# Kernel optimization log

Measured on AMD Instinct MI355X. Metric: run time of the kernel, lower is better.

Reference implementation:

```python
import jax, jax.numpy as jnp
import numpy as np
import math

D_MODEL = 1024
D_STATE = 16
D_CONV = 4
EXPAND = 2
D_INNER = EXPAND * D_MODEL
DT_RANK = math.ceil(D_MODEL / 16)
EPS = 1e-5


def setup_inputs() -> dict:
    key = jax.random.key(0)
    ks = jax.random.split(key, 8)
    B, L = 2, 1024
    s = 0.02
    return {
        "hidden_states": jax.random.normal(ks[0], (B, L, D_MODEL), jnp.float32),
        "norm_weight": jnp.ones((D_MODEL,), jnp.float32),
        "in_proj_w": (jax.random.normal(ks[1], (2 * D_INNER, D_MODEL), jnp.float32) * s),
        "conv_w": (jax.random.normal(ks[2], (D_INNER, D_CONV), jnp.float32) * s),
        "conv_b": jnp.zeros((D_INNER,), jnp.float32),
        "x_proj_w": (jax.random.normal(ks[3], (DT_RANK + 2 * D_STATE, D_INNER), jnp.float32) * s),
        "dt_proj_w": (jax.random.normal(ks[4], (D_INNER, DT_RANK), jnp.float32) * s),
        "dt_proj_b": jax.random.uniform(ks[5], (D_INNER,), jnp.float32, -4.0, -2.0),
        "A_log": jnp.log(jnp.broadcast_to(jnp.arange(1, D_STATE + 1, dtype=jnp.float32), (D_INNER, D_STATE))),
        "D": jnp.ones((D_INNER,), jnp.float32),
        "out_proj_w": (jax.random.normal(ks[6], (D_MODEL, D_INNER), jnp.float32) * s),
    }


def _rmsnorm(x, w):
    # Faithful to source: rms = ||x||_2 / sqrt(d); x / (rms + eps) * w
    norm = jnp.linalg.norm(x, axis=-1, keepdims=True)
    rms = norm * (1.0 / math.sqrt(x.shape[-1]))
    return w * (x / (rms + EPS))


def _mamba(h, in_proj_w, conv_w, conv_b, x_proj_w, dt_proj_w, dt_proj_b, A_log, D, out_proj_w):
    B, L, _ = h.shape
    xz = h @ in_proj_w.T                      # (B,L,2*D_INNER)
    x, z = jnp.split(xz, 2, axis=-1)          # each (B,L,D_INNER)

    # causal depthwise conv1d along L, kernel D_CONV
    xpad = jnp.pad(x, ((0, 0), (D_CONV - 1, 0), (0, 0)))
    xc = conv_b
    for k in range(D_CONV):                   # tiny fixed loop over kernel taps
        xc = xc + xpad[:, k:k + L, :] * conv_w[:, k]
    xc = jax.nn.silu(xc)                      # (B,L,D_INNER)

    x_dbl = xc @ x_proj_w.T                   # (B,L,DT_RANK+2N)
    dt, Bm, Cm = jnp.split(x_dbl, [DT_RANK, DT_RANK + D_STATE], axis=-1)
    dt = jax.nn.softplus(dt @ dt_proj_w.T + dt_proj_b)   # (B,L,D_INNER)

    A = -jnp.exp(A_log)                       # (D_INNER,N)
    deltaA = jnp.exp(dt[..., None] * A)                      # (B,L,D_INNER,N)
    deltaBu = (dt * xc)[..., None] * Bm[:, :, None, :]        # (B,L,D_INNER,N)

    def step(hst, inp):
        dA, dBu, Ct = inp
        hst = dA * hst + dBu                  # (B,D_INNER,N)
        y = jnp.einsum('bdn,bn->bd', hst, Ct)
        return hst, y

    h0 = jnp.zeros((B, D_INNER, D_STATE), xc.dtype)
    _, ys = jax.lax.scan(step, h0, (deltaA.swapaxes(0, 1), deltaBu.swapaxes(0, 1), Cm.swapaxes(0, 1)))
    y = ys.swapaxes(0, 1)                     # (B,L,D_INNER)
    y = y + D * xc
    y = y * jax.nn.silu(z)
    return y @ out_proj_w.T                   # (B,L,D_MODEL)


def reference(hidden_states, norm_weight, in_proj_w, conv_w, conv_b, x_proj_w,
              dt_proj_w, dt_proj_b, A_log, D, out_proj_w):
    residual = hidden_states
    h = _rmsnorm(residual, norm_weight)
    out = _mamba(h, in_proj_w, conv_w, conv_b, x_proj_w, dt_proj_w, dt_proj_b,
                 A_log, D, out_proj_w)
    return out, residual
```

## Files before the change

kernel.cpp:

```cpp
#include <hip/hip_runtime.h>

typedef __bf16 bf16x8 __attribute__((ext_vector_type(8)));
typedef float f32x4 __attribute__((ext_vector_type(4)));

__device__ __forceinline__ float b2f(ushort u) {
    union { unsigned int i; float f; } v;
    v.i = ((unsigned int)u) << 16;
    return v.f;
}
__device__ __forceinline__ ushort f2b(float f) {
    union { float f; unsigned int i; } v;
    v.f = f;
    unsigned int x = v.i;
    unsigned int r = (x + 0x7fffu + ((x >> 16) & 1u)) >> 16;
    return (ushort)r;
}
__device__ __forceinline__ float fexp2(float x) {
#if __has_builtin(__builtin_amdgcn_exp2f)
    return __builtin_amdgcn_exp2f(x);
#else
    return exp2f(x);
#endif
}
__device__ __forceinline__ void gload16(const ushort* g, ushort* l) {
    __builtin_amdgcn_global_load_lds(
        (const __attribute__((address_space(1))) unsigned int*)g,
        (__attribute__((address_space(3))) unsigned int*)l, 16, 0, 0);
}
__device__ __forceinline__ bf16x8 ldsfrag(const ushort* s, int row, int cq) {
    int p = cq ^ (row & 7);
    return *(const bf16x8*)(s + row * 64 + p * 8);
}

#define D_MODEL 1024
#define D_INNER 2048
#define D_STATE 16
#define DT_RANK 64
#define NTOK    2048
#define LSEQ    1024
#define NCH     64
#define LC      16
#define KSL     16
#define LOG2E   1.44269504088896f

__global__ __launch_bounds__(256) void prep_kernel(
    const float* __restrict__ hs, const float* __restrict__ w,
    ushort* __restrict__ hout, float* __restrict__ resid,
    const float* __restrict__ inproj, const float* __restrict__ outproj,
    const float* __restrict__ xprojw, const float* __restrict__ dtw,
    ushort* __restrict__ wIn, ushort* __restrict__ wOut,
    ushort* __restrict__ xpw, ushort* __restrict__ dtwb,
    float* __restrict__ xdbl)
{
    int blk = blockIdx.x;
    int tid = threadIdx.x;
    if (blk < NTOK) {
        int t = blk;
        float4 r4 = *(const float4*)(hs + (size_t)t * D_MODEL + tid * 4);
        float s = r4.x * r4.x + r4.y * r4.y + r4.z * r4.z + r4.w * r4.w;
        #pragma unroll
        for (int off = 32; off >= 1; off >>= 1) s += __shfl_xor(s, off);
        __shared__ float red[4];
        int lane = tid & 63, wid = tid >> 6;
        if (lane == 0) red[wid] = s;
        __syncthreads();
        float tot = red[0] + red[1] + red[2] + red[3];
        float inv = 1.0f / (sqrtf(tot) * (1.0f / 32.0f) + 1e-5f);
        float4 w4 = *(const float4*)(w + tid * 4);
        ushort4 o;
        o.x = f2b(w4.x * r4.x * inv);
        o.y = f2b(w4.y * r4.y * inv);
        o.z = f2b(w4.z * r4.z * inv);
        o.w = f2b(w4.w * r4.w * inv);
        *(ushort4*)(hout + (size_t)t * D_MODEL + tid * 4) = o;
        *(float4*)(resid + (size_t)t * D_MODEL + tid * 4) = r4;
    } else if (blk < NTOK + 6464) {
        int i = (blk - NTOK) * 256 + tid;
        const float* src; ushort* dst; int off;
        if (i < 1048576)      { src = inproj;  dst = wIn;  off = i; }
        else if (i < 1572864) { src = outproj; dst = wOut; off = i - 1048576; }
        else if (i < 1622016) { src = xprojw;  dst = xpw;  off = i - 1572864; }
        else if (i < 1654784) { src = dtw;     dst = dtwb; off = i - 1622016; }
        else return;
        float4 v = *(const float4*)(src + (size_t)off * 4);
        ushort4 o;
        o.x = f2b(v.x); o.y = f2b(v.y); o.z = f2b(v.z); o.w = f2b(v.w);
        *(ushort4*)(dst + (size_t)off * 4) = o;
    } else {
        int i = (blk - NTOK - 6464) * 256 + tid;
        if (i < 49152)
            *(float4*)(xdbl + (size_t)i * 4) = (float4){0.f, 0.f, 0.f, 0.f};
    }
}

__global__ __launch_bounds__(256) void gemm_xz_kernel(
    const ushort* __restrict__ Ag, const ushort* __restrict__ Wg,
    ushort* __restrict__ xq, ushort* __restrict__ zq, int K)
{
    __shared__ __align__(16) ushort smem[128 * 128];
    ushort* sA = smem;
    ushort* sB = smem + 128 * 64;
    int tid = threadIdx.x;
    int bm = blockIdx.x, bn = blockIdx.y;
    int wid = tid >> 6, lane = tid & 63;
    int wm = (wid >> 1) * 64, wn = (wid & 1) * 64;
    int l16 = lane & 15, q = lane >> 4;

    f32x4 acc[4][4];
    #pragma unroll
    for (int i = 0; i < 4; i++)
        #pragma unroll
        for (int j = 0; j < 4; j++)
            acc[i][j] = (f32x4){0.f, 0.f, 0.f, 0.f};

    const ushort* Abase = Ag + (size_t)bm * 128 * K;
    const ushort* Wbase = Wg + (size_t)bn * 128 * K;

    int segr = lane >> 3, segc = lane & 7;
    size_t goff[4]; int sseg[4];
    #pragma unroll
    for (int t = 0; t < 4; t++) {
        int s = wid * 4 + t;
        int r = s * 8 + segr;
        int gc = segc ^ (r & 7);
        sseg[t] = s * 512;
        goff[t] = (size_t)r * K + gc * 8;
    }

    for (int k0 = 0; k0 < K; k0 += 64) {
        __syncthreads();
        #pragma unroll
        for (int t = 0; t < 4; t++) {
            gload16(Abase + goff[t] + k0, sA + sseg[t]);
            gload16(Wbase + goff[t] + k0, sB + sseg[t]);
        }
        __syncthreads();
        #pragma unroll
        for (int ks = 0; ks < 2; ks++) {
            int cq = ks * 4 + q;
            bf16x8 af[4], bfr[4];
            #pragma unroll
            for (int i = 0; i < 4; i++)
                af[i] = ldsfrag(sA, wm + i * 16 + l16, cq);
            #pragma unroll
            for (int j = 0; j < 4; j++)
                bfr[j] = ldsfrag(sB, wn + j * 16 + l16, cq);
            #pragma unroll
            for (int i = 0; i < 4; i++)
                #pragma unroll
                for (int j = 0; j < 4; j++)
                    acc[i][j] = __builtin_amdgcn_mfma_f32_16x16x32_bf16(af[i], bfr[j], acc[i][j], 0, 0, 0);
        }
    }

    __syncthreads();
    #pragma unroll
    for (int i = 0; i < 4; i++)
        #pragma unroll
        for (int j = 0; j < 4; j++) {
            int col = wn + j * 16 + l16;
            int cchunk = col >> 3, cin = col & 7;
            #pragma unroll
            for (int r = 0; r < 4; r++) {
                int row = wm + i * 16 + q * 4 + r;
                smem[row * 128 + ((cchunk ^ (row & 7)) << 3) + cin] =
                    f2b(acc[i][j][r]);
            }
        }
    __syncthreads();
    ushort* dst = (bn < 16) ? xq : zq;
    int colbase = (bn & 15) * 128;
    size_t rowbase = (size_t)bm * 128;
    #pragma unroll
    for (int it = 0; it < 8; it++) {
        int flat = it * 2048 + tid * 8;
        int row = flat >> 7, cchunk = (flat & 127) >> 3;
        *(uint4*)(dst + (rowbase + row) * D_INNER + colbase + (cchunk << 3)) =
            *(const uint4*)(smem + row * 128 + ((cchunk ^ (row & 7)) << 3));
    }
}

__global__ __launch_bounds__(256) void gemm64_kernel(
    const ushort* __restrict__ Ag, const ushort* __restrict__ Wg,
    float* __restrict__ Cf, int M, int N, int K)
{
    __shared__ __align__(16) ushort smem[64 * 128];
    ushort* sA = smem;
    ushort* sB = smem + 64 * 64;
    float* fs = (float*)smem;
    int tid = threadIdx.x;
    int bm = blockIdx.x, bn = blockIdx.y;
    int wid = tid >> 6, lane = tid & 63;
    int wm = wid * 16;
    int l16 = lane & 15, q = lane >> 4;

    f32x4 acc[4];
    #pragma unroll
    for (int j = 0; j < 4; j++) acc[j] = (f32x4){0.f, 0.f, 0.f, 0.f};

    const ushort* Abase = Ag + (size_t)bm * 64 * K;
    const ushort* Wbase = Wg + (size_t)bn * 64 * K;

    int segr = lane >> 3, segc = lane & 7;
    size_t goff[2]; int sseg[2];
    #pragma unroll
    for (int t = 0; t < 2; t++) {
        int s = wid * 2 + t;
        int r = s * 8 + segr;
        int gc = segc ^ (r & 7);
        sseg[t] = s * 512;
        goff[t] = (size_t)r * K + gc * 8;
    }

    for (int k0 = 0; k0 < K; k0 += 64) {
        __syncthreads();
        #pragma unroll
        for (int t = 0; t < 2; t++) {
            gload16(Abase + goff[t] + k0, sA + sseg[t]);
            gload16(Wbase + goff[t] + k0, sB + sseg[t]);
        }
        __syncthreads();
        #pragma unroll
        for (int ks = 0; ks < 2; ks++) {
            int cq = ks * 4 + q;
            bf16x8 af = ldsfrag(sA, wm + l16, cq);
            bf16x8 bfr[4];
            #pragma unroll
            for (int j = 0; j < 4; j++)
                bfr[j] = ldsfrag(sB, j * 16 + l16, cq);
            #pragma unroll
            for (int j = 0; j < 4; j++)
                acc[j] = __builtin_amdgcn_mfma_f32_16x16x32_bf16(af, bfr[j], acc[j], 0, 0, 0);
        }
    }

    __syncthreads();
    #pragma unroll
    for (int j = 0; j < 4; j++)
        #pragma unroll
        for (int r = 0; r < 4; r++)
            fs[(wm + q * 4 + r) * 64 + j * 16 + l16] = acc[j][r];
    __syncthreads();
    #pragma unroll
    for (int it = 0; it < 4; it++) {
        int flat = it * 1024 + tid * 4;
        int row = flat >> 6, col = flat & 63;
        *(float4*)(Cf + (size_t)(bm * 64 + row) * N + bn * 64 + col) =
            *(const float4*)(fs + row * 64 + col);
    }
}

__global__ __launch_bounds__(256) void conv_silu_kernel(
    const ushort* __restrict__ xq, const float* __restrict__ cw,
    const float* __restrict__ cb, ushort* __restrict__ xcb)
{
    int t = blockIdx.x;
    int d0 = threadIdx.x * 8;
    int l = t & (LSEQ - 1), b = t >> 10;

    ushort v[4][8];
    bool has[4];
    #pragma unroll
    for (int k = 0; k < 4; k++) {
        int ll = l - 3 + k;
        has[k] = (ll >= 0);
        if (has[k])
            *(uint4*)v[k] = *(const uint4*)(xq + (((size_t)(b * LSEQ + ll)) << 11) + d0);
    }
    ushort o[8];
    #pragma unroll
    for (int j = 0; j < 8; j++) {
        float4 w4 = *(const float4*)(cw + (size_t)(d0 + j) * 4);
        float wk[4] = {w4.x, w4.y, w4.z, w4.w};
        float acc = cb[d0 + j];
        #pragma unroll
        for (int k = 0; k < 4; k++)
            if (has[k]) acc += b2f(v[k][j]) * wk[k];
        o[j] = f2b(acc / (1.f + __expf(-acc)));
    }
    *(uint4*)(xcb + (((size_t)t) << 11) + d0) = *(const uint4*)o;
}

__global__ __launch_bounds__(256) void xproj_partial_kernel(
    const ushort* __restrict__ xcb, const ushort* __restrict__ wq,
    float* __restrict__ xdbl)
{
    __shared__ __align__(16) ushort sA[128 * 40];
    __shared__ __align__(16) ushort sB[96 * 40];
    int tid = threadIdx.x;
    int bm = blockIdx.x, sl = blockIdx.y;
    int wid = tid >> 6, lane = tid & 63;
    int wm = wid * 32;
    int l16 = lane & 15, q = lane >> 4;

    f32x4 acc[2][6];
    #pragma unroll
    for (int i = 0; i < 2; i++)
        #pragma unroll
        for (int j = 0; j < 6; j++)
            acc[i][j] = (f32x4){0.f, 0.f, 0.f, 0.f};

    const ushort* Abase = xcb + (size_t)bm * 128 * D_INNER;
    int kbase = sl * (D_INNER / KSL);

    for (int kk = 0; kk < D_INNER / KSL; kk += 32) {
        int k0 = kbase + kk;
        __syncthreads();
        #pragma unroll
        for (int i = tid; i < 512; i += 256) {
            int r = i >> 2, c = (i & 3) << 3;
            *(uint4*)(sA + r * 40 + c) = *(const uint4*)(Abase + (size_t)r * D_INNER + k0 + c);
        }
        for (int i = tid; i < 384; i += 256) {
            int r = i >> 2, c = (i & 3) << 3;
            *(uint4*)(sB + r * 40 + c) = *(const uint4*)(wq + (size_t)r * D_INNER + k0 + c);
        }
        __syncthreads();
        bf16x8 af[2], bfr[6];
        #pragma unroll
        for (int i = 0; i < 2; i++)
            af[i] = *(const bf16x8*)(sA + (wm + i * 16 + l16) * 40 + q * 8);
        #pragma unroll
        for (int j = 0; j < 6; j++)
            bfr[j] = *(const bf16x8*)(sB + (j * 16 + l16) * 40 + q * 8);
        #pragma unroll
        for (int i = 0; i < 2; i++)
            #pragma unroll
            for (int j = 0; j < 6; j++)
                acc[i][j] = __builtin_amdgcn_mfma_f32_16x16x32_bf16(af[i], bfr[j], acc[i][j], 0, 0, 0);
    }

    int row0 = bm * 128 + wm + q * 4;
    #pragma unroll
    for (int i = 0; i < 2; i++)
        #pragma unroll
        for (int j = 0; j < 6; j++)
            #pragma unroll
            for (int r = 0; r < 4; r++)
                atomicAdd(&xdbl[(size_t)(row0 + i * 16 + r) * 96 + j * 16 + l16],
                          acc[i][j][r]);
}

__global__ __launch_bounds__(256) void dt_gemm_kernel(
    const float* __restrict__ xdbl, const ushort* __restrict__ dtwq,
    const float* __restrict__ dtb, ushort* __restrict__ dtout)
{
    __shared__ __align__(16) ushort sA[64 * 72];
    __shared__ __align__(16) ushort sB[64 * 72];
    int tid = threadIdx.x;
    int bm = blockIdx.x, bn = blockIdx.y;
    int wid = tid >> 6, lane = tid & 63;
    int wm = wid * 16;
    int l16 = lane & 15, q = lane >> 4;

    const float* Abase = xdbl + (size_t)bm * 64 * 96;
    const ushort* Bbase = dtwq + (size_t)bn * 64 * DT_RANK;
    #pragma unroll
    for (int i = tid; i < 512; i += 256) {
        int r = i >> 3, c = (i & 7) << 3;
        float4 v0 = *(const float4*)(Abase + (size_t)r * 96 + c);
        float4 v1 = *(const float4*)(Abase + (size_t)r * 96 + c + 4);
        ushort o[8] = {f2b(v0.x), f2b(v0.y), f2b(v0.z), f2b(v0.w),
                       f2b(v1.x), f2b(v1.y), f2b(v1.z), f2b(v1.w)};
        *(uint4*)(sA + r * 72 + c) = *(const uint4*)o;
        *(uint4*)(sB + r * 72 + c) = *(const uint4*)(Bbase + (size_t)r * DT_RANK + c);
    }
    __syncthreads();

    f32x4 acc[4];
    #pragma unroll
    for (int j = 0; j < 4; j++) acc[j] = (f32x4){0.f, 0.f, 0.f, 0.f};

    #pragma unroll
    for (int ks = 0; ks < 2; ks++) {
        bf16x8 af = *(const bf16x8*)(sA + (wm + l16) * 72 + ks * 32 + q * 8);
        bf16x8 bfr[4];
        #pragma unroll
        for (int j = 0; j < 4; j++)
            bfr[j] = *(const bf16x8*)(sB + (j * 16 + l16) * 72 + ks * 32 + q * 8);
        #pragma unroll
        for (int j = 0; j < 4; j++)
            acc[j] = __builtin_amdgcn_mfma_f32_16x16x32_bf16(af, bfr[j], acc[j], 0, 0, 0);
    }

    __syncthreads();
    #pragma unroll
    for (int j = 0; j < 4; j++) {
        float bias = dtb[bn * 64 + j * 16 + l16];
        #pragma unroll
        for (int r = 0; r < 4; r++) {
            float s = acc[j][r] + bias;
            float sp = (s > 20.f) ? s : log1pf(__expf(s));
            sA[(wm + q * 4 + r) * 72 + j * 16 + l16] = f2b(sp);
        }
    }
    __syncthreads();
    int row0 = bm * 64, col0 = bn * 64;
    #pragma unroll
    for (int rep = 0; rep < 2; rep++) {
        int off = rep * 2048 + tid * 8;
        int row = off >> 6, col = off & 63;
        *(uint4*)(dtout + (size_t)(row0 + row) * D_INNER + col0 + col) =
            *(const uint4*)(sA + row * 72 + col);
    }
}

__global__ __launch_bounds__(256) void scan_partA_kernel(
    const ushort* __restrict__ dt, const ushort* __restrict__ xcq,
    const float* __restrict__ xdbl, const float* __restrict__ Alog,
    float2* __restrict__ ch)
{
    __shared__ float sBC[LC][32];
    int bid = blockIdx.x;
    int g = bid & 7;
    int c = (bid >> 3) & (NCH - 1);
    int b = bid >> 9;
    int tid = threadIdx.x;
    int lane = tid & 63, wid = tid >> 6;
    int d = g * 256 + wid * 64 + lane;
    int l0 = c * LC;

    if (tid < LC * 8) {
        int r = tid >> 3, c4 = (tid & 7) * 4;
        *(float4*)&sBC[r][c4] =
            *(const float4*)(xdbl + ((size_t)(b * LSEQ + l0 + r)) * 96 + 64 + c4);
    }
    float A[16];
    #pragma unroll
    for (int k = 0; k < 4; k++)
        *(float4*)&A[k * 4] = *(const float4*)(Alog + d * D_STATE + k * 4);
    #pragma unroll
    for (int n = 0; n < 16; n++) A[n] = -__expf(A[n]) * LOG2E;
    __syncthreads();

    const ushort* dtp = dt  + ((size_t)(b * LSEQ + l0)) * D_INNER + d;
    const ushort* xcp = xcq + ((size_t)(b * LSEQ + l0)) * D_INNER + d;

    float h[16], ap[16];
    #pragma unroll
    for (int n = 0; n < 16; n++) { h[n] = 0.f; ap[n] = 1.f; }

    for (int l = 0; l < LC; l++) {
        float dtv = b2f(dtp[(size_t)l * D_INNER]);
        float xcv = b2f(xcp[(size_t)l * D_INNER]);
        float t = dtv * xcv;
        float Bv[16];
        #pragma unroll
        for (int k = 0; k < 4; k++)
            *(float4*)&Bv[k * 4] = *(const float4*)&sBC[l][k * 4];
        #pragma unroll
        for (int n = 0; n < 16; n++) {
            float a = fexp2(dtv * A[n]);
            h[n] = h[n] * a + t * Bv[n];
            ap[n] *= a;
        }
    }

    float2* outp = ch + (((size_t)(c * 2 + b)) << 15) + (d << 4);
    #pragma unroll
    for (int n = 0; n < 16; n += 2) {
        float4 v = {ap[n], h[n], ap[n + 1], h[n + 1]};
        *(float4*)&outp[n] = v;
    }
}

__global__ __launch_bounds__(256) void scan_partB_kernel(
    const float2* __restrict__ ch, float* __restrict__ hinit)
{
    int kk = blockIdx.x * 256 + threadIdx.x;
    int b = kk >> 15, dn = kk & 32767;
    float run = 0.f;
    #pragma unroll 8
    for (int c = 0; c < NCH; c++) {
        size_t off = (((size_t)(c * 2 + b)) << 15) + dn;
        float2 v = ch[off];
        hinit[off] = run;
        run = v.x * run + v.y;
    }
}

__global__ __launch_bounds__(256) void scan_partC_kernel(
    const ushort* __restrict__ dt, const ushort* __restrict__ xcq,
    const float* __restrict__ xdbl, const ushort* __restrict__ zq,
    const float* __restrict__ Alog, const float* __restrict__ Dp,
    const float* __restrict__ hinit, ushort* __restrict__ yg)
{
    __shared__ float sBC[LC][32];
    int bid = blockIdx.x;
    int g = bid & 7;
    int c = (bid >> 3) & (NCH - 1);
    int b = bid >> 9;
    int tid = threadIdx.x;
    int lane = tid & 63, wid = tid >> 6;
    int d = g * 256 + wid * 64 + lane;
    int l0 = c * LC;

    if (tid < LC * 8) {
        int r = tid >> 3, c4 = (tid & 7) * 4;
        *(float4*)&sBC[r][c4] =
            *(const float4*)(xdbl + ((size_t)(b * LSEQ + l0 + r)) * 96 + 64 + c4);
    }
    float A[16];
    #pragma unroll
    for (int k = 0; k < 4; k++)
        *(float4*)&A[k * 4] = *(const float4*)(Alog + d * D_STATE + k * 4);
    #pragma unroll
    for (int n = 0; n < 16; n++) A[n] = -__expf(A[n]) * LOG2E;
    float Dd = Dp[d];

    const float* hp = hinit + (((size_t)(c * 2 + b)) << 15) + (d << 4);
    float h[16];
    #pragma unroll
    for (int n = 0; n < 16; n += 4)
        *(float4*)&h[n] = *(const float4*)(hp + n);
    __syncthreads();

    const ushort* dtp = dt  + ((size_t)(b * LSEQ + l0)) * D_INNER + d;
    const ushort* xcp = xcq + ((size_t)(b * LSEQ + l0)) * D_INNER + d;
    const ushort* zp  = zq  + ((size_t)(b * LSEQ + l0)) * D_INNER + d;
    ushort* yp = yg + ((size_t)(b * LSEQ + l0)) * D_INNER + d;

    for (int l = 0; l < LC; l++) {
        float dtv = b2f(dtp[(size_t)l * D_INNER]);
        float xcv = b2f(xcp[(size_t)l * D_INNER]);
        float zv  = b2f(zp[(size_t)l * D_INNER]);
        float t = dtv * xcv;
        float Bv[16], Cv[16];
        #pragma unroll
        for (int k = 0; k < 4; k++) {
            *(float4*)&Bv[k * 4] = *(const float4*)&sBC[l][k * 4];
            *(float4*)&Cv[k * 4] = *(const float4*)&sBC[l][16 + k * 4];
        }
        float p0 = 0.f, p1 = 0.f, p2 = 0.f, p3 = 0.f;
        #pragma unroll
        for (int n = 0; n < 16; n += 4) {
            float a0 = fexp2(dtv * A[n]);
            float a1 = fexp2(dtv * A[n + 1]);
            float a2 = fexp2(dtv * A[n + 2]);
            float a3 = fexp2(dtv * A[n + 3]);
            h[n]     = h[n] * a0 + t * Bv[n];
            h[n + 1] = h[n + 1] * a1 + t * Bv[n + 1];
            h[n + 2] = h[n + 2] * a2 + t * Bv[n + 2];
            h[n + 3] = h[n + 3] * a3 + t * Bv[n + 3];
            p0 += h[n] * Cv[n];
            p1 += h[n + 1] * Cv[n + 1];
            p2 += h[n + 2] * Cv[n + 2];
            p3 += h[n + 3] * Cv[n + 3];
        }
        float p = (p0 + p1) + (p2 + p3);
        float y = p + Dd * xcv;
        float sz = zv / (1.f + __expf(-zv));
        yp[(size_t)l * D_INNER] = f2b(y * sz);
    }
}

extern "C" void kernel_launch(void* const* d_in, const int* in_sizes, int n_in,
                              void* d_out, int out_size, void* d_ws, size_t ws_size,
                              hipStream_t stream)
{
    const float* hs      = (const float*)d_in[0];
    const float* norm_w  = (const float*)d_in[1];
    const float* inproj  = (const float*)d_in[2];
    const float* convw   = (const float*)d_in[3];
    const float* convb   = (const float*)d_in[4];
    const float* xprojw  = (const float*)d_in[5];
    const float* dtw     = (const float*)d_in[6];
    const float* dtb     = (const float*)d_in[7];
    const float* alog    = (const float*)d_in[8];
    const float* dvec    = (const float*)d_in[9];
    const float* outproj = (const float*)d_in[10];

    float* out_main  = (float*)d_out;
    float* out_resid = (float*)d_out + (size_t)NTOK * D_MODEL;

    char* ws = (char*)d_ws;
    ushort* xq      = (ushort*)(ws);
    ushort* zq      = (ushort*)(ws +  8388608);
    ushort* dtq     = (ushort*)(ws + 16777216);
    ushort* xcb     = (ushort*)(ws + 25165824);
    float2* ch      = (float2*)(ws + 33554432);
    float*  xdbl    = (float*) (ws + 67108864);
    ushort* wIn     = (ushort*)(ws + 67895296);
    ushort* wOut    = (ushort*)(ws + 76283904);
    ushort* h_bf16  = (ushort*)(ws + 80478208);
    ushort* xpw_b   = (ushort*)(ws + 84672512);
    ushort* dtw_b   = (ushort*)(ws + 85065728);
    ushort* yg_bf16 = (ushort*)(ws + 85327872);
    float*  hinit   = (float*) (ws + 93716480);

    prep_kernel<<<NTOK + 6464 + 192, 256, 0, stream>>>(
        hs, norm_w, h_bf16, out_resid,
        inproj, outproj, xprojw, dtw, wIn, wOut, xpw_b, dtw_b, xdbl);

    gemm_xz_kernel<<<dim3(NTOK / 128, (2 * D_INNER) / 128), 256, 0, stream>>>(
        h_bf16, wIn, xq, zq, D_MODEL);

    conv_silu_kernel<<<NTOK, 256, 0, stream>>>(xq, convw, convb, xcb);

    xproj_partial_kernel<<<dim3(NTOK / 128, KSL), 256, 0, stream>>>(
        xcb, xpw_b, xdbl);

    dt_gemm_kernel<<<dim3(NTOK / 64, D_INNER / 64), 256, 0, stream>>>(
        xdbl, dtw_b, dtb, dtq);

    scan_partA_kernel<<<1024, 256, 0, stream>>>(dtq, xcb, xdbl, alog, ch);
    scan_partB_kernel<<<256, 256, 0, stream>>>(ch, hinit);
    scan_partC_kernel<<<1024, 256, 0, stream>>>(dtq, xcb, xdbl, zq,
                                                alog, dvec, hinit, yg_bf16);

    gemm64_kernel<<<dim3(NTOK / 64, D_MODEL / 64), 256, 0, stream>>>(
        yg_bf16, wOut, out_main, NTOK, D_MODEL, D_INNER);
}
```

Before: 261.9 us.

## Pack chunk scan carries to bf16 and derive decay product from summed dt

```diff
diff --git a/kernel.cpp b/kernel.cpp
--- a/kernel.cpp
+++ b/kernel.cpp
@@ -21,6 +21,9 @@
 #else
     return exp2f(x);
 #endif
+}
+__device__ __forceinline__ unsigned int packb2(float ap, float h) {
+    return ((unsigned int)f2b(h) << 16) | (unsigned int)f2b(ap);
 }
 __device__ __forceinline__ void gload16(const ushort* g, ushort* l) {
     __builtin_amdgcn_global_load_lds(
@@ -408,7 +411,7 @@
 __global__ __launch_bounds__(256) void scan_partA_kernel(
     const ushort* __restrict__ dt, const ushort* __restrict__ xcq,
     const float* __restrict__ xdbl, const float* __restrict__ Alog,
-    float2* __restrict__ ch)
+    unsigned int* __restrict__ ch)
 {
     __shared__ float sBC[LC][32];
     int bid = blockIdx.x;
@@ -436,14 +439,16 @@
     const ushort* dtp = dt  + ((size_t)(b * LSEQ + l0)) * D_INNER + d;
     const ushort* xcp = xcq + ((size_t)(b * LSEQ + l0)) * D_INNER + d;
 
-    float h[16], ap[16];
-    #pragma unroll
-    for (int n = 0; n < 16; n++) { h[n] = 0.f; ap[n] = 1.f; }
+    float h[16];
+    #pragma unroll
+    for (int n = 0; n < 16; n++) h[n] = 0.f;
+    float S = 0.f;
 
     for (int l = 0; l < LC; l++) {
         float dtv = b2f(dtp[(size_t)l * D_INNER]);
         float xcv = b2f(xcp[(size_t)l * D_INNER]);
         float t = dtv * xcv;
+        S += dtv;
         float Bv[16];
         #pragma unroll
         for (int k = 0; k < 4; k++)
@@ -452,20 +457,23 @@
         for (int n = 0; n < 16; n++) {
             float a = fexp2(dtv * A[n]);
             h[n] = h[n] * a + t * Bv[n];
-            ap[n] *= a;
-        }
-    }
-
-    float2* outp = ch + (((size_t)(c * 2 + b)) << 15) + (d << 4);
-    #pragma unroll
-    for (int n = 0; n < 16; n += 2) {
-        float4 v = {ap[n], h[n], ap[n + 1], h[n + 1]};
-        *(float4*)&outp[n] = v;
+        }
+    }
+
+    unsigned int* outp = ch + (((size_t)(c * 2 + b)) << 15) + (d << 4);
+    #pragma unroll
+    for (int n = 0; n < 16; n += 4) {
+        uint4 v;
+        v.x = packb2(fexp2(A[n] * S),     h[n]);
+        v.y = packb2(fexp2(A[n + 1] * S), h[n + 1]);
+        v.z = packb2(fexp2(A[n + 2] * S), h[n + 2]);
+        v.w = packb2(fexp2(A[n + 3] * S), h[n + 3]);
+        *(uint4*)&outp[n] = v;
     }
 }
 
 __global__ __launch_bounds__(256) void scan_partB_kernel(
-    const float2* __restrict__ ch, float* __restrict__ hinit)
+    const unsigned int* __restrict__ ch, ushort* __restrict__ hinit)
 {
     int kk = blockIdx.x * 256 + threadIdx.x;
     int b = kk >> 15, dn = kk & 32767;
@@ -473,9 +481,9 @@
     #pragma unroll 8
     for (int c = 0; c < NCH; c++) {
         size_t off = (((size_t)(c * 2 + b)) << 15) + dn;
-        float2 v = ch[off];
-        hinit[off] = run;
-        run = v.x * run + v.y;
+        unsigned int v = ch[off];
+        hinit[off] = f2b(run);
+        run = b2f((ushort)(v & 0xffffu)) * run + b2f((ushort)(v >> 16));
     }
 }
 
@@ -483,7 +491,7 @@
     const ushort* __restrict__ dt, const ushort* __restrict__ xcq,
     const float* __restrict__ xdbl, const ushort* __restrict__ zq,
     const float* __restrict__ Alog, const float* __restrict__ Dp,
-    const float* __restrict__ hinit, ushort* __restrict__ yg)
+    const ushort* __restrict__ hinit, ushort* __restrict__ yg)
 {
     __shared__ float sBC[LC][32];
     int bid = blockIdx.x;
@@ -508,11 +516,14 @@
     for (int n = 0; n < 16; n++) A[n] = -__expf(A[n]) * LOG2E;
     float Dd = Dp[d];
 
-    const float* hp = hinit + (((size_t)(c * 2 + b)) << 15) + (d << 4);
+    const ushort* hp = hinit + (((size_t)(c * 2 + b)) << 15) + (d << 4);
     float h[16];
     #pragma unroll
-    for (int n = 0; n < 16; n += 4)
-        *(float4*)&h[n] = *(const float4*)(hp + n);
+    for (int n = 0; n < 16; n += 4) {
+        ushort4 v = *(const ushort4*)(hp + n);
+        h[n] = b2f(v.x); h[n + 1] = b2f(v.y);
+        h[n + 2] = b2f(v.z); h[n + 3] = b2f(v.w);
+    }
     __syncthreads();
 
     const ushort* dtp = dt  + ((size_t)(b * LSEQ + l0)) * D_INNER + d;
@@ -574,19 +585,19 @@
     float* out_resid = (float*)d_out + (size_t)NTOK * D_MODEL;
 
     char* ws = (char*)d_ws;
-    ushort* xq      = (ushort*)(ws);
-    ushort* zq      = (ushort*)(ws +  8388608);
-    ushort* dtq     = (ushort*)(ws + 16777216);
-    ushort* xcb     = (ushort*)(ws + 25165824);
-    float2* ch      = (float2*)(ws + 33554432);
-    float*  xdbl    = (float*) (ws + 67108864);
-    ushort* wIn     = (ushort*)(ws + 67895296);
-    ushort* wOut    = (ushort*)(ws + 76283904);
-    ushort* h_bf16  = (ushort*)(ws + 80478208);
-    ushort* xpw_b   = (ushort*)(ws + 84672512);
-    ushort* dtw_b   = (ushort*)(ws + 85065728);
-    ushort* yg_bf16 = (ushort*)(ws + 85327872);
-    float*  hinit   = (float*) (ws + 93716480);
+    ushort*       xq    = (ushort*)(ws);
+    ushort*       zq    = (ushort*)(ws +  8388608);
+    ushort*       dtq   = (ushort*)(ws + 16777216);
+    ushort*       xcb   = (ushort*)(ws + 25165824);
+    unsigned int* ch    = (unsigned int*)(ws + 33554432);
+    ushort*       hinit = (ushort*)(ws + 50331648);
+    float*        xdbl  = (float*) (ws + 67108864);
+    ushort*       wIn   = (ushort*)(ws + 67895296);
+    ushort*       wOut  = (ushort*)(ws + 76283904);
+    ushort*       h_bf16= (ushort*)(ws + 80478208);
+    ushort*       xpw_b = (ushort*)(ws + 84672512);
+    ushort*       dtw_b = (ushort*)(ws + 85065728);
+    ushort*       yg_bf16=(ushort*)(ws + 85327872);
 
     prep_kernel<<<NTOK + 6464 + 192, 256, 0, stream>>>(
         hs, norm_w, h_bf16, out_resid,
```

After: 251.3 us. -4.0%, faster.
